# Optimization experiments

Hardware: AMD Instinct MI355X
Metric: run time of the kernel (lower is better)

Reference implementation:

```python
import jax, jax.numpy as jnp
import numpy as np

N, D, H = 100000, 128, 8
C = D // H
E = 800000
NEG_SLOPE = 0.2


def setup_inputs() -> dict:
    key = jax.random.key(0)
    k1, k2, k3, k4, k5, k6 = jax.random.split(key, 6)
    x = jax.random.normal(k1, (N, D), dtype=jnp.float32)
    edge_index = jax.random.randint(k2, (2, E), 0, N, dtype=jnp.int64)
    # GATConv params: shared linear (single node-feature input), per-head attention vectors, bias
    W = jax.random.normal(k3, (D, H * C), dtype=jnp.float32) * (1.0 / np.sqrt(D))
    att_src = jax.random.normal(k4, (H, C), dtype=jnp.float32) * 0.1
    att_dst = jax.random.normal(k5, (H, C), dtype=jnp.float32) * 0.1
    bias = jnp.zeros((H * C,), dtype=jnp.float32)
    return {"x": x, "edge_index": edge_index, "W": W, "att_src": att_src, "att_dst": att_dst, "bias": bias}


def reference(x, edge_index, W, att_src, att_dst, bias):
    # PyG GATConv default: add self-loops
    loops = jnp.tile(jnp.arange(N, dtype=edge_index.dtype), (2, 1))  # [2, N]
    ei = jnp.concatenate([edge_index, loops], axis=1)                # [2, E+N]
    src, dst = ei[0], ei[1]

    h = (x @ W).reshape(N, H, C)                    # [N, H, C]
    a_src = jnp.einsum('nhc,hc->nh', h, att_src)    # [N, H]
    a_dst = jnp.einsum('nhc,hc->nh', h, att_dst)    # [N, H]

    logits = jax.nn.leaky_relu(a_src[src] + a_dst[dst], negative_slope=NEG_SLOPE)  # [Etot, H]

    # segment softmax grouped by destination node (every node has a self-loop -> non-empty)
    mx = jax.ops.segment_max(logits, dst, num_segments=N)   # [N, H]
    ex = jnp.exp(logits - mx[dst])                           # [Etot, H]
    denom = jax.ops.segment_sum(ex, dst, num_segments=N)    # [N, H]
    alpha = ex / (denom[dst] + 1e-16)                        # [Etot, H]

    msg = h[src] * alpha[:, :, None]                         # [Etot, H, C]
    out = jax.ops.segment_sum(msg, dst, num_segments=N)      # [N, H, C]
    out = out.reshape(N, H * C) + bias                       # concat heads
    return out, ei, alpha
```

## Files before the change

kernel.cpp:

```cpp
#include <hip/hip_runtime.h>
#include <hip/hip_bf16.h>
#include <cstdint>

#define N_NODES 100000
#define DIM 128
#define HEADS 8
#define CH 16
#define NEDGE 800000
#define ETOT (NEDGE + N_NODES)
#define NEG_SLOPE 0.2f
#define CAP 32
#define PRE 16

typedef __attribute__((ext_vector_type(8))) short bf16x8;
typedef __attribute__((ext_vector_type(4))) float f32x4;

__device__ __forceinline__ float leaky(float v) {
    return v >= 0.f ? v : NEG_SLOPE * v;
}

__device__ __forceinline__ void wave_lds_fence() {
    asm volatile("s_waitcnt lgkmcnt(0)" ::: "memory");
    __builtin_amdgcn_sched_barrier(0);
}

__device__ __forceinline__ void split2(float w, ushort& hi, ushort& lo) {
    __hip_bfloat16 bh = __float2bfloat16(w);
    float r = w - __bfloat162float(bh);
    __hip_bfloat16 bl = __float2bfloat16(r);
    hi = *(ushort*)&bh;
    lo = *(ushort*)&bl;
}

__device__ __forceinline__ ushort bf16hi(float w) {
    __hip_bfloat16 bh = __float2bfloat16(w);
    return *(ushort*)&bh;
}

#define NCOLS 144
#define LDK   136
#define MT    128
#define GEMM_BLOCKS ((N_NODES + MT - 1) / MT)
#define EPB  1536

__global__ __launch_bounds__(512, 8) void fused_kernel(
    const float* __restrict__ x, const float* __restrict__ W,
    const float* __restrict__ att_src, const float* __restrict__ att_dst,
    __hip_bfloat16* __restrict__ h, float* __restrict__ a_src,
    float* __restrict__ a_dst,
    const int* __restrict__ edge_index, float* __restrict__ ei_out,
    int* __restrict__ fill, int2* __restrict__ ebuf2)
{
    __shared__ ushort Whi[NCOLS * LDK];
    const int tid = threadIdx.x;
    const int bid = blockIdx.x;

    int ee[3], es[3], ed[3];
    #pragma unroll
    for (int t = 0; t < 3; ++t) {
        const int e = bid * EPB + t * 512 + tid;
        ee[t] = e;
        if (e < ETOT) {
            if (e < NEDGE) { es[t] = edge_index[e]; ed[t] = edge_index[NEDGE + e]; }
            else           { es[t] = ed[t] = e - NEDGE; }
        }
    }
    int pos[3];
    #pragma unroll
    for (int t = 0; t < 3; ++t) {
        if (ee[t] < ETOT) {
            ei_out[ee[t]]        = (float)es[t];
            ei_out[ETOT + ee[t]] = (float)ed[t];
            pos[t] = atomicAdd(&fill[ed[t]], 1);
        }
    }

    {
        const int n  = tid >> 2;
        const int kq = (tid & 3) * 32;
        #pragma unroll
        for (int j = 0; j < 32; j += 2) {
            const int k = kq + j;
            float w0 = W[(size_t)k * DIM + n];
            float w1 = W[(size_t)(k + 1) * DIM + n];
            *(uint*)&Whi[n * LDK + k] = (uint)bf16hi(w0) | ((uint)bf16hi(w1) << 16);
        }
    }
    if (tid < 64) {
        const int t  = tid >> 2;
        const int kq = (tid & 3) * 32;
        const int hd = t & 7;
        const float* av = ((t < 8) ? att_src : att_dst) + hd * CH;
        float avr[CH];
        #pragma unroll
        for (int c = 0; c < CH; ++c) avr[c] = av[c];
        const int nrow = 128 + t;
        for (int j = 0; j < 32; j += 2) {
            const int k = kq + j;
            const float* wp0 = &W[(size_t)k * DIM + hd * CH];
            const float* wp1 = wp0 + DIM;
            float s0 = 0.f, s1 = 0.f;
            #pragma unroll
            for (int c = 0; c < CH; ++c) { s0 += wp0[c] * avr[c]; s1 += wp1[c] * avr[c]; }
            *(uint*)&Whi[nrow * LDK + k] = (uint)bf16hi(s0) | ((uint)bf16hi(s1) << 16);
        }
    }

    #pragma unroll
    for (int t = 0; t < 3; ++t) {
        if (ee[t] < ETOT && pos[t] < CAP)
            ebuf2[ed[t] * CAP + pos[t]] = make_int2(ee[t], es[t]);
    }
    __syncthreads();

    const int w    = tid >> 6;
    const int lane = tid & 63;
    const int r    = lane & 15;
    const int g    = lane >> 4;
    const long arow = (long)bid * MT + w * 16 + r;
    const bool avalid = arow < N_NODES;

    f32x4 acc[9] = {};
    #pragma unroll
    for (int ks = 0; ks < 4; ++ks) {
        const int k0 = ks * 32 + g * 8;
        float xv[8];
        if (avalid) {
            *(float4*)&xv[0] = *(const float4*)&x[arow * DIM + k0];
            *(float4*)&xv[4] = *(const float4*)&x[arow * DIM + k0 + 4];
        } else {
            #pragma unroll
            for (int j = 0; j < 8; ++j) xv[j] = 0.f;
        }
        bf16x8 ahi, alo;
        #pragma unroll
        for (int j = 0; j < 8; ++j) {
            ushort hb, lb;
            split2(xv[j], hb, lb);
            ahi[j] = (short)hb;
            alo[j] = (short)lb;
        }
        #pragma unroll
        for (int nt = 0; nt < 9; ++nt) {
            const int nr = nt * 16 + r;
            bf16x8 bhi = *(const bf16x8*)&Whi[nr * LDK + k0];
            acc[nt] = __builtin_amdgcn_mfma_f32_16x16x32_bf16(ahi, bhi, acc[nt], 0, 0, 0);
            acc[nt] = __builtin_amdgcn_mfma_f32_16x16x32_bf16(alo, bhi, acc[nt], 0, 0, 0);
        }
    }

    const long orow0 = (long)bid * MT + w * 16 + g * 4;
    #pragma unroll
    for (int q = 0; q < 4; ++q) {
        const long orow = orow0 + q;
        if (orow < N_NODES) {
            #pragma unroll
            for (int nt = 0; nt < 8; ++nt)
                h[orow * DIM + nt * 16 + r] = __float2bfloat16(acc[nt][q]);
            const float av = acc[8][q];
            if (r < 8) a_src[orow * HEADS + r]       = av;
            else       a_dst[orow * HEADS + (r - 8)] = av;
        }
    }
}

__global__ __launch_bounds__(256) void gather_kernel(
    const int* __restrict__ fill, const int2* __restrict__ ebuf2,
    const __hip_bfloat16* __restrict__ h,
    const float* __restrict__ a_src, const float* __restrict__ a_dst,
    const float* __restrict__ bias, float* __restrict__ alpha_out,
    float* __restrict__ out)
{
    __shared__ int2  s_es[4][CAP];
    __shared__ float s_al[4][CAP][9];
    const int tid  = threadIdx.x;
    const int w    = tid >> 6;
    const int lane = tid & 63;
    const int n    = blockIdx.x * 4 + w;
    const int head = lane >> 3, c = lane & 7;
    const int chb  = head * CH + c * 2;
    const int dn   = min(fill[n], CAP);
    const float ad = a_dst[(uint)n * HEADS + head];

    if (lane < dn)
        s_es[w][lane] = ebuf2[(uint)n * CAP + lane];
    wave_lds_fence();

    const char* asb = (const char*)a_src;
    const uint  hdo = (uint)(head << 2);
    int   sidx[4];
    float asv[4];
    #pragma unroll
    for (int k = 0; k < 4; ++k) {
        const int i = c + 8 * k;
        if (i < dn) {
            sidx[k] = s_es[w][i].y;
            asv[k]  = *(const float*)(asb + ((uint)sidx[k] * 32u + hdo));
        }
    }

    const char* hb  = (const char*)h;
    const uint  cho = (uint)chb * 2u;
    const int npre = min(dn, PRE);
    unsigned hv[PRE];
    #pragma unroll
    for (int q = 0; q < PRE; ++q) {
        if (q < npre)
            hv[q] = *(const unsigned*)(hb + ((uint)s_es[w][q].y * 256u + cho));
    }

    float lg[4];
    float m = -1e30f;
    #pragma unroll
    for (int k = 0; k < 4; ++k) {
        const int i = c + 8 * k;
        if (i < dn) {
            lg[k] = leaky(asv[k] + ad);
            m = fmaxf(m, lg[k]);
        }
    }
    #pragma unroll
    for (int off = 1; off < 8; off <<= 1)
        m = fmaxf(m, __shfl_xor(m, off));

    float dsum = 0.f;
    #pragma unroll
    for (int k = 0; k < 4; ++k) {
        const int i = c + 8 * k;
        if (i < dn) {
            float ex = __expf(lg[k] - m);
            s_al[w][i][head] = ex;
            dsum += ex;
        }
    }
    #pragma unroll
    for (int off = 1; off < 8; off <<= 1)
        dsum += __shfl_xor(dsum, off);
    const float rdinv = 1.f / (dsum + 1e-16f);
    wave_lds_fence();

    float ax = 0.f, ay = 0.f;
    #pragma unroll
    for (int q = 0; q < PRE; ++q) {
        if (q < npre) {
            float ex = s_al[w][q][head];
            ax += __uint_as_float(hv[q] << 16) * ex;
            ay += __uint_as_float(hv[q] & 0xffff0000u) * ex;
        }
    }
    for (int i = PRE; i < dn; ++i) {
        unsigned hq = *(const unsigned*)(hb + ((uint)s_es[w][i].y * 256u + cho));
        float ex = s_al[w][i][head];
        ax += __uint_as_float(hq << 16) * ex;
        ay += __uint_as_float(hq & 0xffff0000u) * ex;
    }
    ax *= rdinv; ay *= rdinv;
    float2 b = *(const float2*)&bias[chb];
    float2 r; r.x = ax + b.x; r.y = ay + b.y;
    *(float2*)&out[(uint)n * DIM + chb] = r;

    for (int i = c; i < dn; i += 8)
        alpha_out[(uint)s_es[w][i].x * 8u + head] = s_al[w][i][head] * rdinv;
}

extern "C" void kernel_launch(void* const* d_in, const int* in_sizes, int n_in,
                              void* d_out, int out_size, void* d_ws, size_t ws_size,
                              hipStream_t stream) {
    const float* x          = (const float*)d_in[0];
    const int*   edge_index = (const int*)d_in[1];
    const float* W          = (const float*)d_in[2];
    const float* att_src    = (const float*)d_in[3];
    const float* att_dst    = (const float*)d_in[4];
    const float* bias       = (const float*)d_in[5];

    float* out       = (float*)d_out;
    float* ei_out    = out + (size_t)N_NODES * DIM;
    float* alpha_out = ei_out + 2 * (size_t)ETOT;

    __hip_bfloat16* h = (__hip_bfloat16*)d_ws;
    float* a_src = (float*)(h + (size_t)N_NODES * DIM);
    float* a_dst = a_src + (size_t)N_NODES * HEADS;
    int*   fill  = (int*)(a_dst + (size_t)N_NODES * HEADS);
    int2*  ebuf2 = (int2*)(fill + N_NODES);

    hipMemsetAsync(fill, 0, (size_t)N_NODES * sizeof(int), stream);

    fused_kernel<<<GEMM_BLOCKS, 512, 0, stream>>>(
        x, W, att_src, att_dst, h, a_src, a_dst,
        edge_index, ei_out, fill, ebuf2);
    gather_kernel<<<N_NODES / 4, 256, 0, stream>>>(fill, ebuf2, h,
                                                   a_src, a_dst, bias, alpha_out, out);
}
```

Measured before the change: 288.0 us.

## Add W low-part bf16 pass and halve GEMM rows per block

The fused GEMM tile shrinks from 128 to 64 rows per block, and edges per block drop to match. The 8 waves now split into 4 row groups times 2 column groups. A second pass rebuilds the shared W tile with the bf16 residual of W and multiplies it by the high part of x, adding a third split-bf16 product (xhi*Wlo) for accuracy. The cost is extra MFMA work, a second W staging with two more barriers, and a redundant W conversion in each of roughly twice as many blocks.

```diff
diff --git a/kernel.cpp b/kernel.cpp
--- a/kernel.cpp
+++ b/kernel.cpp
@@ -31,17 +31,22 @@
     hi = *(ushort*)&bh;
     lo = *(ushort*)&bl;
 }
-
 __device__ __forceinline__ ushort bf16hi(float w) {
     __hip_bfloat16 bh = __float2bfloat16(w);
     return *(ushort*)&bh;
 }
+__device__ __forceinline__ ushort bf16lo(float w) {
+    __hip_bfloat16 bh = __float2bfloat16(w);
+    float r = w - __bfloat162float(bh);
+    __hip_bfloat16 bl = __float2bfloat16(r);
+    return *(ushort*)&bl;
+}
 
 #define NCOLS 144
 #define LDK   136
-#define MT    128
+#define MT    64
 #define GEMM_BLOCKS ((N_NODES + MT - 1) / MT)
-#define EPB  1536
+#define EPB   576
 
 __global__ __launch_bounds__(512, 8) void fused_kernel(
     const float* __restrict__ x, const float* __restrict__ W,
@@ -51,26 +56,29 @@
     const int* __restrict__ edge_index, float* __restrict__ ei_out,
     int* __restrict__ fill, int2* __restrict__ ebuf2)
 {
-    __shared__ ushort Whi[NCOLS * LDK];
+    __shared__ ushort Wt[NCOLS * LDK];
     const int tid = threadIdx.x;
     const int bid = blockIdx.x;
 
-    int ee[3], es[3], ed[3];
-    #pragma unroll
-    for (int t = 0; t < 3; ++t) {
-        const int e = bid * EPB + t * 512 + tid;
-        ee[t] = e;
-        if (e < ETOT) {
+    int es[2], ed[2];
+    bool ev[2];
+    #pragma unroll
+    for (int t = 0; t < 2; ++t) {
+        const int off = t * 512 + tid;
+        const int e = bid * EPB + off;
+        ev[t] = (off < EPB) && (e < ETOT);
+        if (ev[t]) {
             if (e < NEDGE) { es[t] = edge_index[e]; ed[t] = edge_index[NEDGE + e]; }
             else           { es[t] = ed[t] = e - NEDGE; }
         }
     }
-    int pos[3];
-    #pragma unroll
-    for (int t = 0; t < 3; ++t) {
-        if (ee[t] < ETOT) {
-            ei_out[ee[t]]        = (float)es[t];
-            ei_out[ETOT + ee[t]] = (float)ed[t];
+    int pos[2];
+    #pragma unroll
+    for (int t = 0; t < 2; ++t) {
+        if (ev[t]) {
+            const int e = bid * EPB + t * 512 + tid;
+            ei_out[e]        = (float)es[t];
+            ei_out[ETOT + e] = (float)ed[t];
             pos[t] = atomicAdd(&fill[ed[t]], 1);
         }
     }
@@ -83,7 +91,7 @@
             const int k = kq + j;
             float w0 = W[(size_t)k * DIM + n];
             float w1 = W[(size_t)(k + 1) * DIM + n];
-            *(uint*)&Whi[n * LDK + k] = (uint)bf16hi(w0) | ((uint)bf16hi(w1) << 16);
+            *(uint*)&Wt[n * LDK + k] = (uint)bf16hi(w0) | ((uint)bf16hi(w1) << 16);
         }
     }
     if (tid < 64) {
@@ -102,14 +110,14 @@
             float s0 = 0.f, s1 = 0.f;
             #pragma unroll
             for (int c = 0; c < CH; ++c) { s0 += wp0[c] * avr[c]; s1 += wp1[c] * avr[c]; }
-            *(uint*)&Whi[nrow * LDK + k] = (uint)bf16hi(s0) | ((uint)bf16hi(s1) << 16);
-        }
-    }
-
-    #pragma unroll
-    for (int t = 0; t < 3; ++t) {
-        if (ee[t] < ETOT && pos[t] < CAP)
-            ebuf2[ed[t] * CAP + pos[t]] = make_int2(ee[t], es[t]);
+            *(uint*)&Wt[nrow * LDK + k] = (uint)bf16hi(s0) | ((uint)bf16hi(s1) << 16);
+        }
+    }
+
+    #pragma unroll
+    for (int t = 0; t < 2; ++t) {
+        if (ev[t] && pos[t] < CAP)
+            ebuf2[ed[t] * CAP + pos[t]] = make_int2(bid * EPB + t * 512 + tid, es[t]);
     }
     __syncthreads();
 
@@ -117,10 +125,12 @@
     const int lane = tid & 63;
     const int r    = lane & 15;
     const int g    = lane >> 4;
-    const long arow = (long)bid * MT + w * 16 + r;
+    const int rg   = w >> 1, cg = w & 1;
+    const long arow = (long)bid * MT + rg * 16 + r;
     const bool avalid = arow < N_NODES;
 
-    f32x4 acc[9] = {};
+    f32x4 acc[5] = {};
+
     #pragma unroll
     for (int ks = 0; ks < 4; ++ks) {
         const int k0 = ks * 32 + g * 8;
@@ -141,25 +151,89 @@
             alo[j] = (short)lb;
         }
         #pragma unroll
-        for (int nt = 0; nt < 9; ++nt) {
-            const int nr = nt * 16 + r;
-            bf16x8 bhi = *(const bf16x8*)&Whi[nr * LDK + k0];
-            acc[nt] = __builtin_amdgcn_mfma_f32_16x16x32_bf16(ahi, bhi, acc[nt], 0, 0, 0);
-            acc[nt] = __builtin_amdgcn_mfma_f32_16x16x32_bf16(alo, bhi, acc[nt], 0, 0, 0);
-        }
-    }
-
-    const long orow0 = (long)bid * MT + w * 16 + g * 4;
+        for (int j = 0; j < 5; ++j) {
+            const int nt = 2 * j + cg;
+            if (nt < 9) {
+                bf16x8 b = *(const bf16x8*)&Wt[(nt * 16 + r) * LDK + k0];
+                acc[j] = __builtin_amdgcn_mfma_f32_16x16x32_bf16(ahi, b, acc[j], 0, 0, 0);
+                acc[j] = __builtin_amdgcn_mfma_f32_16x16x32_bf16(alo, b, acc[j], 0, 0, 0);
+            }
+        }
+    }
+
+    __syncthreads();
+    {
+        const int n  = tid >> 2;
+        const int kq = (tid & 3) * 32;
+        #pragma unroll
+        for (int j = 0; j < 32; j += 2) {
+            const int k = kq + j;
+            float w0 = W[(size_t)k * DIM + n];
+            float w1 = W[(size_t)(k + 1) * DIM + n];
+            *(uint*)&Wt[n * LDK + k] = (uint)bf16lo(w0) | ((uint)bf16lo(w1) << 16);
+        }
+    }
+    if (tid < 64) {
+        const int t  = tid >> 2;
+        const int kq = (tid & 3) * 32;
+        const int hd = t & 7;
+        const float* av = ((t < 8) ? att_src : att_dst) + hd * CH;
+        float avr[CH];
+        #pragma unroll
+        for (int c = 0; c < CH; ++c) avr[c] = av[c];
+        const int nrow = 128 + t;
+        for (int j = 0; j < 32; j += 2) {
+            const int k = kq + j;
+            const float* wp0 = &W[(size_t)k * DIM + hd * CH];
+            const float* wp1 = wp0 + DIM;
+            float s0 = 0.f, s1 = 0.f;
+            #pragma unroll
+            for (int c = 0; c < CH; ++c) { s0 += wp0[c] * avr[c]; s1 += wp1[c] * avr[c]; }
+            *(uint*)&Wt[nrow * LDK + k] = (uint)bf16lo(s0) | ((uint)bf16lo(s1) << 16);
+        }
+    }
+    __syncthreads();
+
+    #pragma unroll
+    for (int ks = 0; ks < 4; ++ks) {
+        const int k0 = ks * 32 + g * 8;
+        float xv[8];
+        if (avalid) {
+            *(float4*)&xv[0] = *(const float4*)&x[arow * DIM + k0];
+            *(float4*)&xv[4] = *(const float4*)&x[arow * DIM + k0 + 4];
+        } else {
+            #pragma unroll
+            for (int j = 0; j < 8; ++j) xv[j] = 0.f;
+        }
+        bf16x8 ahi;
+        #pragma unroll
+        for (int j = 0; j < 8; ++j) ahi[j] = (short)bf16hi(xv[j]);
+        #pragma unroll
+        for (int j = 0; j < 5; ++j) {
+            const int nt = 2 * j + cg;
+            if (nt < 9) {
+                bf16x8 b = *(const bf16x8*)&Wt[(nt * 16 + r) * LDK + k0];
+                acc[j] = __builtin_amdgcn_mfma_f32_16x16x32_bf16(ahi, b, acc[j], 0, 0, 0);
+            }
+        }
+    }
+
+    const long orow0 = (long)bid * MT + rg * 16 + g * 4;
     #pragma unroll
     for (int q = 0; q < 4; ++q) {
         const long orow = orow0 + q;
         if (orow < N_NODES) {
             #pragma unroll
-            for (int nt = 0; nt < 8; ++nt)
-                h[orow * DIM + nt * 16 + r] = __float2bfloat16(acc[nt][q]);
-            const float av = acc[8][q];
-            if (r < 8) a_src[orow * HEADS + r]       = av;
-            else       a_dst[orow * HEADS + (r - 8)] = av;
+            for (int j = 0; j < 5; ++j) {
+                const int nt = 2 * j + cg;
+                if (nt < 8)
+                    h[orow * DIM + nt * 16 + r] = __float2bfloat16(acc[j][q]);
+            }
+            if (cg == 0) {
+                const float av = acc[4][q];
+                if (r < 8) a_src[orow * HEADS + r]       = av;
+                else       a_dst[orow * HEADS + (r - 8)] = av;
+            }
         }
     }
 }
@@ -188,15 +262,12 @@
 
     const char* asb = (const char*)a_src;
     const uint  hdo = (uint)(head << 2);
-    int   sidx[4];
     float asv[4];
     #pragma unroll
     for (int k = 0; k < 4; ++k) {
         const int i = c + 8 * k;
-        if (i < dn) {
-            sidx[k] = s_es[w][i].y;
-            asv[k]  = *(const float*)(asb + ((uint)sidx[k] * 32u + hdo));
-        }
+        if (i < dn)
+            asv[k] = *(const float*)(asb + ((uint)s_es[w][i].y * 32u + hdo));
     }
 
     const char* hb  = (const char*)h;
```

After: 547.7 us. 1.9x slower.

## Precompute MFMA-fragment-ordered split-bf16 weights in a prep kernel, drop LDS staging

Applied to the files above, without the earlier changes.

A new prep kernel converts W and the folded attention columns into hi/lo bf16 pairs, stored in the exact per-lane MFMA fragment order. The fused kernel then reads B fragments straight from global memory (L2-resident) instead of rebuilding the W tile in LDS in every block, which also removes the __syncthreads. Blocks shrink to 256 threads with 64 rows and 576 edges each. A third MFMA (ahi*blo) is added to improve precision. This costs an extra kernel launch and more MFMA and global-load work per block.

```diff
diff --git a/kernel.cpp b/kernel.cpp
--- a/kernel.cpp
+++ b/kernel.cpp
@@ -32,35 +32,65 @@
     lo = *(ushort*)&bl;
 }
 
-__device__ __forceinline__ ushort bf16hi(float w) {
-    __hip_bfloat16 bh = __float2bfloat16(w);
-    return *(ushort*)&bh;
-}
-
-#define NCOLS 144
-#define LDK   136
-#define MT    128
+__global__ __launch_bounds__(256) void prep_kernel(
+    const float* __restrict__ W, const float* __restrict__ att_src,
+    const float* __restrict__ att_dst,
+    ushort* __restrict__ fragHi, ushort* __restrict__ fragLo)
+{
+    const int b   = blockIdx.x;
+    const int nt  = b >> 2, ks = b & 3;
+    const int tid = threadIdx.x;
+    const int lane = tid >> 2;
+    const int j0   = (tid & 3) * 2;
+    const int r = lane & 15, g = lane >> 4;
+    const int k0 = ks * 32 + g * 8;
+    #pragma unroll
+    for (int u = 0; u < 2; ++u) {
+        const int j = j0 + u;
+        const int k = k0 + j;
+        float val;
+        if (nt < 8) {
+            val = W[(size_t)k * DIM + nt * 16 + r];
+        } else {
+            const int hd = r & 7;
+            const float* av = ((r < 8) ? att_src : att_dst) + hd * CH;
+            const float* wp = &W[(size_t)k * DIM + hd * CH];
+            float s = 0.f;
+            #pragma unroll
+            for (int c = 0; c < CH; ++c) s += wp[c] * av[c];
+            val = s;
+        }
+        const size_t idx = ((size_t)(nt * 4 + ks) * 64 + lane) * 8 + j;
+        ushort hi, lo;
+        split2(val, hi, lo);
+        fragHi[idx] = hi;
+        fragLo[idx] = lo;
+    }
+}
+
+#define MT 64
 #define GEMM_BLOCKS ((N_NODES + MT - 1) / MT)
-#define EPB  1536
-
-__global__ __launch_bounds__(512, 8) void fused_kernel(
-    const float* __restrict__ x, const float* __restrict__ W,
-    const float* __restrict__ att_src, const float* __restrict__ att_dst,
+#define EPB 576
+
+__global__ __launch_bounds__(256) void fused_kernel(
+    const float* __restrict__ x,
+    const ushort* __restrict__ fragHi, const ushort* __restrict__ fragLo,
     __hip_bfloat16* __restrict__ h, float* __restrict__ a_src,
     float* __restrict__ a_dst,
     const int* __restrict__ edge_index, float* __restrict__ ei_out,
     int* __restrict__ fill, int2* __restrict__ ebuf2)
 {
-    __shared__ ushort Whi[NCOLS * LDK];
     const int tid = threadIdx.x;
     const int bid = blockIdx.x;
 
-    int ee[3], es[3], ed[3];
+    int es[3], ed[3];
+    bool ev[3];
     #pragma unroll
     for (int t = 0; t < 3; ++t) {
-        const int e = bid * EPB + t * 512 + tid;
-        ee[t] = e;
-        if (e < ETOT) {
+        const int off = t * 256 + tid;
+        const int e = bid * EPB + off;
+        ev[t] = (off < EPB) && (e < ETOT);
+        if (ev[t]) {
             if (e < NEDGE) { es[t] = edge_index[e]; ed[t] = edge_index[NEDGE + e]; }
             else           { es[t] = ed[t] = e - NEDGE; }
         }
@@ -68,50 +98,18 @@
     int pos[3];
     #pragma unroll
     for (int t = 0; t < 3; ++t) {
-        if (ee[t] < ETOT) {
-            ei_out[ee[t]]        = (float)es[t];
-            ei_out[ETOT + ee[t]] = (float)ed[t];
+        if (ev[t]) {
+            const int e = bid * EPB + t * 256 + tid;
+            ei_out[e]        = (float)es[t];
+            ei_out[ETOT + e] = (float)ed[t];
             pos[t] = atomicAdd(&fill[ed[t]], 1);
         }
     }
-
-    {
-        const int n  = tid >> 2;
-        const int kq = (tid & 3) * 32;
-        #pragma unroll
-        for (int j = 0; j < 32; j += 2) {
-            const int k = kq + j;
-            float w0 = W[(size_t)k * DIM + n];
-            float w1 = W[(size_t)(k + 1) * DIM + n];
-            *(uint*)&Whi[n * LDK + k] = (uint)bf16hi(w0) | ((uint)bf16hi(w1) << 16);
-        }
-    }
-    if (tid < 64) {
-        const int t  = tid >> 2;
-        const int kq = (tid & 3) * 32;
-        const int hd = t & 7;
-        const float* av = ((t < 8) ? att_src : att_dst) + hd * CH;
-        float avr[CH];
-        #pragma unroll
-        for (int c = 0; c < CH; ++c) avr[c] = av[c];
-        const int nrow = 128 + t;
-        for (int j = 0; j < 32; j += 2) {
-            const int k = kq + j;
-            const float* wp0 = &W[(size_t)k * DIM + hd * CH];
-            const float* wp1 = wp0 + DIM;
-            float s0 = 0.f, s1 = 0.f;
-            #pragma unroll
-            for (int c = 0; c < CH; ++c) { s0 += wp0[c] * avr[c]; s1 += wp1[c] * avr[c]; }
-            *(uint*)&Whi[nrow * LDK + k] = (uint)bf16hi(s0) | ((uint)bf16hi(s1) << 16);
-        }
-    }
-
     #pragma unroll
     for (int t = 0; t < 3; ++t) {
-        if (ee[t] < ETOT && pos[t] < CAP)
-            ebuf2[ed[t] * CAP + pos[t]] = make_int2(ee[t], es[t]);
-    }
-    __syncthreads();
+        if (ev[t] && pos[t] < CAP)
+            ebuf2[ed[t] * CAP + pos[t]] = make_int2(bid * EPB + t * 256 + tid, es[t]);
+    }
 
     const int w    = tid >> 6;
     const int lane = tid & 63;
@@ -119,6 +117,8 @@
     const int g    = lane >> 4;
     const long arow = (long)bid * MT + w * 16 + r;
     const bool avalid = arow < N_NODES;
+    const ushort* fH = fragHi + (size_t)lane * 8;
+    const ushort* fL = fragLo + (size_t)lane * 8;
 
     f32x4 acc[9] = {};
     #pragma unroll
@@ -142,10 +142,12 @@
         }
         #pragma unroll
         for (int nt = 0; nt < 9; ++nt) {
-            const int nr = nt * 16 + r;
-            bf16x8 bhi = *(const bf16x8*)&Whi[nr * LDK + k0];
+            const size_t fo = (size_t)(nt * 4 + ks) * 512;
+            bf16x8 bhi = *(const bf16x8*)(fH + fo);
+            bf16x8 blo = *(const bf16x8*)(fL + fo);
             acc[nt] = __builtin_amdgcn_mfma_f32_16x16x32_bf16(ahi, bhi, acc[nt], 0, 0, 0);
             acc[nt] = __builtin_amdgcn_mfma_f32_16x16x32_bf16(alo, bhi, acc[nt], 0, 0, 0);
+            acc[nt] = __builtin_amdgcn_mfma_f32_16x16x32_bf16(ahi, blo, acc[nt], 0, 0, 0);
         }
     }
 
@@ -188,15 +190,12 @@
 
     const char* asb = (const char*)a_src;
     const uint  hdo = (uint)(head << 2);
-    int   sidx[4];
     float asv[4];
     #pragma unroll
     for (int k = 0; k < 4; ++k) {
         const int i = c + 8 * k;
-        if (i < dn) {
-            sidx[k] = s_es[w][i].y;
-            asv[k]  = *(const float*)(asb + ((uint)sidx[k] * 32u + hdo));
-        }
+        if (i < dn)
+            asv[k] = *(const float*)(asb + ((uint)s_es[w][i].y * 32u + hdo));
     }
 
     const char* hb  = (const char*)h;
@@ -282,11 +281,14 @@
     float* a_dst = a_src + (size_t)N_NODES * HEADS;
     int*   fill  = (int*)(a_dst + (size_t)N_NODES * HEADS);
     int2*  ebuf2 = (int2*)(fill + N_NODES);
+    ushort* fragHi = (ushort*)(ebuf2 + (size_t)N_NODES * CAP);
+    ushort* fragLo = fragHi + 9 * 4 * 64 * 8;
 
     hipMemsetAsync(fill, 0, (size_t)N_NODES * sizeof(int), stream);
 
-    fused_kernel<<<GEMM_BLOCKS, 512, 0, stream>>>(
-        x, W, att_src, att_dst, h, a_src, a_dst,
+    prep_kernel<<<36, 256, 0, stream>>>(W, att_src, att_dst, fragHi, fragLo);
+    fused_kernel<<<GEMM_BLOCKS, 256, 0, stream>>>(
+        x, fragHi, fragLo, h, a_src, a_dst,
         edge_index, ei_out, fill, ebuf2);
     gather_kernel<<<N_NODES / 4, 256, 0, stream>>>(fill, ebuf2, h,
                                                    a_src, a_dst, bias, alpha_out, out);
```

Result: no change. 287.0 us (-0.3%).
